# Optimization experiments

Hardware: AMD Instinct MI355X
Metric: run time of the kernel (lower is better)

The kernel has to match this reference:

```python
import jax, jax.numpy as jnp
import numpy as np

L_IN, L_K = 1, 1            # degree ranges (0..L)
C_IN, K_CH, H = 16, 8, 4    # in_channels, k_channels (per head), num_heads
C_OUT = H * K_CH            # 32
E, N_NODES, EMB = 32768, 4096, 64
M_IN, M_K = (L_IN + 1) ** 2, (L_K + 1) ** 2


def _so2_pairs(L_in, L_out):
    # enumerate SO(2)-equivariant weight blocks: for each order m, all (l_in, l_out)
    # pairs with l >= m; m=0 uses 1 matrix, m>0 uses 2 (real/imag parts).
    pairs, w = [], 0
    for m in range(min(L_in, L_out) + 1):
        for l_in in range(m, L_in + 1):
            for l_out in range(m, L_out + 1):
                pairs.append((m, l_in, l_out, w))
                w += 1 if m == 0 else 2
    return pairs, w

_PAIRS, NUM_W = _so2_pairs(L_IN, L_K)  # NUM_W = 6 for L_in=L_k=1


def so2_linear(x, W, L_in, L_out):
    # x: [E, (L_in+1)^2, Cin]; W: [NUM_W, Cin, Cout] (shared) or [E, NUM_W, Cin, Cout] (per-edge)
    per_edge = (W.ndim == 4)
    Cout = W.shape[-1]
    out = jnp.zeros((x.shape[0], (L_out + 1) ** 2, Cout), x.dtype)

    def mat(xs, w):
        return jnp.einsum('ec,eco->eo', xs, W[:, w]) if per_edge else xs @ W[w]

    pairs, _ = _so2_pairs(L_in, L_out)
    for m, l_in, l_out, w in pairs:
        i_in, i_out = l_in * (l_in + 1), l_out * (l_out + 1)  # flat index of (l, m=0)
        if m == 0:
            out = out.at[:, i_out].add(mat(x[:, i_in], w))
        else:
            xp, xn = x[:, i_in + m], x[:, i_in - m]
            out = out.at[:, i_out + m].add(mat(xp, w) - mat(xn, w + 1))
            out = out.at[:, i_out - m].add(mat(xp, w + 1) + mat(xn, w))
    return out


def segment_softmax(z, index, num_segments):
    # PyG-style softmax over ragged neighborhoods (max is detached, as in PyG)
    zmax = jax.lax.stop_gradient(jax.ops.segment_max(z, index, num_segments=num_segments))
    e = jnp.exp(z - zmax[index])
    denom = jax.ops.segment_sum(e, index, num_segments=num_segments)
    return e / denom[index]


def setup_inputs() -> dict:
    key = jax.random.key(0)
    ks = jax.random.split(key, 6)
    x_q = jax.random.normal(ks[0], (E, M_IN, C_IN), jnp.float32)
    x_k = jax.random.normal(ks[1], (E, M_IN, C_IN), jnp.float32)
    edge_emb = jax.random.normal(ks[2], (E, EMB), jnp.float32)
    index = jnp.sort(jax.random.randint(ks[3], (E,), 0, N_NODES))
    W_q = jax.random.normal(ks[4], (NUM_W, C_IN, C_OUT), jnp.float32) / np.sqrt(C_IN)
    W_p = jax.random.normal(ks[5], (EMB, NUM_W * C_IN * C_OUT), jnp.float32) / np.sqrt(EMB)
    return {"x_q": x_q, "x_k": x_k, "edge_emb": edge_emb, "index": index,
            "W_q": W_q, "W_p": W_p, "num_nodes": N_NODES}


def reference(x_q, x_k, edge_emb, index, W_q, W_p, num_nodes):
    # q_ij = W_Q x_i ; static SO2 weights
    q = so2_linear(x_q, W_q, L_IN, L_K).reshape(-1, M_K, H, K_CH)
    # k_ij = W_K(||r_ij||) x_j ; per-edge dynamic SO2 weights from edge embedding
    W_k = (edge_emb @ W_p).reshape(-1, NUM_W, C_IN, C_OUT)
    k = so2_linear(x_k, W_k, L_IN, L_K).reshape(-1, M_K, H, K_CH)
    scale = (K_CH // H) ** (-0.5)  # faithful to original: (k_channels // num_heads)**-0.5
    z = (q * k).sum((-1, -3)) * scale  # [E, H]
    return segment_softmax(z, index, num_nodes)
```

## Files before the change

### kernel.cpp

```cpp
#include <hip/hip_runtime.h>
#include <math.h>

#define E_TOTAL 32768
#define NUM_NODES 4096
#define SCALE 0.70710678118654752f

typedef __attribute__((ext_vector_type(8))) short bfrag;
typedef __attribute__((ext_vector_type(16))) float facc;

__device__ inline unsigned short f2bf(float f) {
  unsigned int u = __float_as_uint(f);
  unsigned int r = (u + 0x7FFFu + ((u >> 16) & 1u)) >> 16;
  return (unsigned short)r;
}
__device__ inline float bf2f(unsigned short s) {
  return __uint_as_float(((unsigned int)s) << 16);
}
__device__ inline void cvt8(const float* v, bfrag& hi, bfrag& lo) {
#pragma unroll
  for (int i = 0; i < 8; ++i) {
    unsigned short h = f2bf(v[i]);
    hi[i] = (short)h;
    lo[i] = (short)f2bf(v[i] - bf2f(h));
  }
}

__global__ __launch_bounds__(256) void prep_kernel(
    const float* __restrict__ Wp, const float* __restrict__ Wq,
    const int* __restrict__ index,
    unsigned short* __restrict__ fragWp, unsigned short* __restrict__ fragWq,
    int* __restrict__ offs)
{
  const int b = blockIdx.x, t = threadIdx.x;
  if (b < 96) {
    __shared__ unsigned short lds[4096];
    const int c = b / 6, w = b - c * 6;
    const int colbase = w * 512 + c * 32;
    const int cl = t & 31, dg = t >> 5;
#pragma unroll
    for (int i = 0; i < 8; ++i) {
      const int d = dg * 8 + i;
      const float v = Wp[(size_t)d * 3072 + colbase + cl];
      const unsigned short hi = f2bf(v);
      const unsigned short lo = f2bf(v - bf2f(hi));
      const int ks = d >> 4;
      const int lane = ((d >> 3) & 1) * 32 + cl;
      const int j = d & 7;
      lds[(ks * 2 + 0) * 512 + lane * 8 + j] = hi;
      lds[(ks * 2 + 1) * 512 + lane * 8 + j] = lo;
    }
    __syncthreads();
    unsigned short* dst = fragWp + (size_t)b * 4096;
    ((uint4*)dst)[t] = ((const uint4*)lds)[t];
    ((uint4*)dst)[t + 256] = ((const uint4*)lds)[t + 256];
  } else if (b < 103) {
    const int slot = b - 96;
    const int w = (slot == 6) ? 5 : slot;
    const float sgn = (slot == 6) ? -1.f : 1.f;
    for (int tt = t; tt < 512; tt += 256) {
      const int lane = tt >> 3, j = tt & 7;
      const int o = lane & 31, c = (lane >> 5) * 8 + j;
      const float v = sgn * Wq[(size_t)(w * 16 + c) * 32 + o];
      const unsigned short hi = f2bf(v);
      const unsigned short lo = f2bf(v - bf2f(hi));
      fragWq[slot * 1024 + lane * 8 + j] = hi;
      fragWq[slot * 1024 + 512 + lane * 8 + j] = lo;
    }
  } else {
    const int tg = (b - 103) * 256 + t;
    if (tg >= E_TOTAL) return;
    const int cur = index[tg];
    const int prev = (tg == 0) ? -1 : index[tg - 1];
    for (int n = prev + 1; n <= cur; ++n) offs[n] = tg;
    if (tg == E_TOTAL - 1)
      for (int n = cur + 1; n <= NUM_NODES; ++n) offs[n] = E_TOTAL;
  }
}

__global__ __launch_bounds__(256, 1) void main_kernel(
    const float* __restrict__ x_q, const float* __restrict__ x_k,
    const float* __restrict__ emb,
    const unsigned short* __restrict__ fragWp,
    const unsigned short* __restrict__ fragWq,
    float* __restrict__ z)
{
  __shared__ float xk_t[64][129];

  const int t = threadIdx.x;
  const int lane = t & 63, wv = t >> 6;
  const int col = lane & 31, half = lane >> 5;
  const int eb = blockIdx.x * 128;
  const int el = wv * 32 + col;
  const int e = eb + el;

  {
    const int er = t & 127, dh = (t >> 7) * 32;
    const float* src = x_k + (size_t)(eb + er) * 64 + dh;
#pragma unroll
    for (int i = 0; i < 8; ++i) {
      float4 v = *(const float4*)(src + i * 4);
      xk_t[dh + i * 4 + 0][er] = v.x;
      xk_t[dh + i * 4 + 1][er] = v.y;
      xk_t[dh + i * 4 + 2][er] = v.z;
      xk_t[dh + i * 4 + 3][er] = v.w;
    }
  }

  bfrag ebh[4], ebl[4];
#pragma unroll
  for (int ks = 0; ks < 4; ++ks) {
    float tmp[8];
    *(float4*)&tmp[0] = *(const float4*)(emb + (size_t)e * 64 + ks * 16 + half * 8);
    *(float4*)&tmp[4] = *(const float4*)(emb + (size_t)e * 64 + ks * 16 + half * 8 + 4);
    cvt8(tmp, ebh[ks], ebl[ks]);
  }

  facc ka0 = {0}, ka1 = {0}, ka2 = {0}, ka3 = {0};

  const unsigned short* fbase = fragWp + lane * 8;

  bfrag curh[4], curl[4], nxth[4], nxtl[4];
#pragma unroll
  for (int ks = 0; ks < 4; ++ks) {
    *(uint4*)&curh[ks] = *(const uint4*)(fbase + ks * 1024);
    *(uint4*)&curl[ks] = *(const uint4*)(fbase + ks * 1024 + 512);
  }

  __syncthreads();

  float xkc0 = 0.f, xkc1 = 0.f, xkc2 = 0.f, xkc3 = 0.f;

  for (int ot = 0; ot < 4; ++ot) {
#pragma unroll 6
    for (int ii = 0; ii < 24; ++ii) {
      const int it = ot * 24 + ii;
      const int j = ii % 6;
      {
        const int itn = (it < 95) ? it + 1 : 95;
        const unsigned short* gp = fbase + (size_t)itn * 4096;
#pragma unroll
        for (int ks = 0; ks < 4; ++ks) {
          *(uint4*)&nxth[ks] = *(const uint4*)(gp + ks * 1024);
          *(uint4*)&nxtl[ks] = *(const uint4*)(gp + ks * 1024 + 512);
        }
      }
      if (j == 0) {
        const int c16 = it / 6;
        xkc0 = xk_t[c16][el];
        xkc1 = xk_t[16 + c16][el];
        xkc2 = xk_t[32 + c16][el];
        xkc3 = xk_t[48 + c16][el];
      }
      facc cc0 = {0.f}, cc1 = {0.f}, cc2 = {0.f};
#pragma unroll
      for (int ks = 0; ks < 4; ++ks) {
        cc0 = __builtin_amdgcn_mfma_f32_32x32x16_bf16(curh[ks], ebh[ks], cc0, 0, 0, 0);
        cc1 = __builtin_amdgcn_mfma_f32_32x32x16_bf16(curh[ks], ebl[ks], cc1, 0, 0, 0);
        cc2 = __builtin_amdgcn_mfma_f32_32x32x16_bf16(curl[ks], ebh[ks], cc2, 0, 0, 0);
      }
      if (j < 4) {
        const float xv = (j & 2) ? xkc2 : xkc0;
        facc& kd = (j & 1) ? ka2 : ka0;
#pragma unroll
        for (int r = 0; r < 16; ++r)
          kd[r] = fmaf(xv, cc0[r] + cc1[r] + cc2[r], kd[r]);
      } else if (j == 4) {
#pragma unroll
        for (int r = 0; r < 16; ++r) {
          const float s = cc0[r] + cc1[r] + cc2[r];
          ka1[r] = fmaf(xkc1, s, ka1[r]);
          ka3[r] = fmaf(xkc3, s, ka3[r]);
        }
      } else {
#pragma unroll
        for (int r = 0; r < 16; ++r) {
          const float s = cc0[r] + cc1[r] + cc2[r];
          ka1[r] = fmaf(xkc3, s, ka1[r]);
          ka3[r] = fmaf(-xkc1, s, ka3[r]);
        }
      }
#pragma unroll
      for (int ks = 0; ks < 4; ++ks) { curh[ks] = nxth[ks]; curl[ks] = nxtl[ks]; }
    }
    __syncthreads();
  }

  bfrag xqh[4], xql[4];
#pragma unroll
  for (int a = 0; a < 4; ++a) {
    float tmp[8];
    *(float4*)&tmp[0] = *(const float4*)(x_q + (size_t)e * 64 + a * 16 + half * 8);
    *(float4*)&tmp[4] = *(const float4*)(x_q + (size_t)e * 64 + a * 16 + half * 8 + 4);
    cvt8(tmp, xqh[a], xql[a]);
  }
  float zp0 = 0.f, zp1 = 0.f, zp2 = 0.f, zp3 = 0.f;
  const int QA1[4] = {0, 1, 0, 3}, QS1[4] = {0, 4, 1, 4};
  const int QA2[4] = {2, 3, 2, 1}, QS2[4] = {2, 5, 3, 6};
#pragma unroll
  for (int m = 0; m < 4; ++m) {
    facc qa = {0.f};
#pragma unroll
    for (int tm = 0; tm < 2; ++tm) {
      const int a = tm ? QA2[m] : QA1[m];
      const int sl = tm ? QS2[m] : QS1[m];
      bfrag wh, wl;
      *(uint4*)&wh = *(const uint4*)(fragWq + sl * 1024 + lane * 8);
      *(uint4*)&wl = *(const uint4*)(fragWq + sl * 1024 + 512 + lane * 8);
      qa = __builtin_amdgcn_mfma_f32_32x32x16_bf16(wh, xqh[a], qa, 0, 0, 0);
      qa = __builtin_amdgcn_mfma_f32_32x32x16_bf16(wh, xql[a], qa, 0, 0, 0);
      qa = __builtin_amdgcn_mfma_f32_32x32x16_bf16(wl, xqh[a], qa, 0, 0, 0);
    }
    const facc& km = (m == 0) ? ka0 : (m == 1) ? ka1 : (m == 2) ? ka2 : ka3;
#pragma unroll
    for (int r = 0; r < 16; ++r) {
      const float v = qa[r] * km[r];
      if (r < 4) zp0 += v;
      else if (r < 8) zp1 += v;
      else if (r < 12) zp2 += v;
      else zp3 += v;
    }
  }
  zp0 += __shfl_xor(zp0, 32);
  zp1 += __shfl_xor(zp1, 32);
  zp2 += __shfl_xor(zp2, 32);
  zp3 += __shfl_xor(zp3, 32);
  if (half == 0) {
    float4 v = {zp0 * SCALE, zp1 * SCALE, zp2 * SCALE, zp3 * SCALE};
    *(float4*)&z[(size_t)e * 4] = v;
  }
}

__global__ __launch_bounds__(256) void softmax_kernel(
    const float* __restrict__ z, const int* __restrict__ offs,
    float* __restrict__ out)
{
  const int node = blockIdx.x * 4 + (threadIdx.x >> 6);
  const int lane = threadIdx.x & 63;
  const int start = offs[node], end = offs[node + 1];
  if (start >= end) return;
  const int h = lane & 3, eo = lane >> 2;
  float m = -INFINITY;
  for (int e = start + eo; e < end; e += 16) m = fmaxf(m, z[(size_t)e * 4 + h]);
#pragma unroll
  for (int s = 4; s < 64; s <<= 1) m = fmaxf(m, __shfl_xor(m, s));
  float sum = 0.f;
  for (int e = start + eo; e < end; e += 16) sum += __expf(z[(size_t)e * 4 + h] - m);
#pragma unroll
  for (int s = 4; s < 64; s <<= 1) sum += __shfl_xor(sum, s);
  const float inv = 1.f / sum;
  for (int e = start + eo; e < end; e += 16)
    out[(size_t)e * 4 + h] = __expf(z[(size_t)e * 4 + h] - m) * inv;
}

extern "C" void kernel_launch(void* const* d_in, const int* in_sizes, int n_in,
                              void* d_out, int out_size, void* d_ws, size_t ws_size,
                              hipStream_t stream) {
  const float* x_q = (const float*)d_in[0];
  const float* x_k = (const float*)d_in[1];
  const float* emb = (const float*)d_in[2];
  const int* index = (const int*)d_in[3];
  const float* W_q = (const float*)d_in[4];
  const float* W_p = (const float*)d_in[5];
  float* out = (float*)d_out;

  char* ws = (char*)d_ws;
  float* z = (float*)ws;
  int* offs = (int*)(ws + 524288);
  unsigned short* fragWp = (unsigned short*)(ws + 524288 + 32768);
  unsigned short* fragWq = (unsigned short*)(ws + 524288 + 32768 + 786432);

  prep_kernel<<<231, 256, 0, stream>>>(W_p, W_q, index, fragWp, fragWq, offs);
  main_kernel<<<256, 256, 0, stream>>>(x_q, x_k, emb, fragWp, fragWq, z);
  softmax_kernel<<<1024, 256, 0, stream>>>(z, offs, out);
}
```

Measured before the change: 124.7 us.

## Stage shared weight fragments into a double-buffered LDS via global_load_lds

```diff
diff --git a/kernel.cpp b/kernel.cpp
--- a/kernel.cpp
+++ b/kernel.cpp
@@ -23,6 +23,12 @@
     hi[i] = (short)h;
     lo[i] = (short)f2bf(v[i] - bf2f(h));
   }
+}
+
+__device__ inline void stage16(const void* g, void* l) {
+  __builtin_amdgcn_global_load_lds(
+      (const __attribute__((address_space(1))) unsigned int*)g,
+      (__attribute__((address_space(3))) unsigned int*)l, 16, 0, 0);
 }
 
 __global__ __launch_bounds__(256) void prep_kernel(
@@ -85,6 +91,7 @@
     float* __restrict__ z)
 {
   __shared__ float xk_t[64][129];
+  __shared__ alignas(16) unsigned short wbuf[2][4096];
 
   const int t = threadIdx.x;
   const int lane = t & 63, wv = t >> 6;
@@ -106,6 +113,13 @@
     }
   }
 
+  {
+    const char* tb = (const char*)fragWp;
+    char* db = (char*)&wbuf[0][0];
+    stage16(tb + (wv * 2 + 0) * 1024 + lane * 16, db + (wv * 2 + 0) * 1024);
+    stage16(tb + (wv * 2 + 1) * 1024 + lane * 16, db + (wv * 2 + 1) * 1024);
+  }
+
   bfrag ebh[4], ebl[4];
 #pragma unroll
   for (int ks = 0; ks < 4; ++ks) {
@@ -117,54 +131,47 @@
 
   facc ka0 = {0}, ka1 = {0}, ka2 = {0}, ka3 = {0};
 
-  const unsigned short* fbase = fragWp + lane * 8;
-
-  bfrag curh[4], curl[4], nxth[4], nxtl[4];
-#pragma unroll
-  for (int ks = 0; ks < 4; ++ks) {
-    *(uint4*)&curh[ks] = *(const uint4*)(fbase + ks * 1024);
-    *(uint4*)&curl[ks] = *(const uint4*)(fbase + ks * 1024 + 512);
-  }
-
   __syncthreads();
 
   float xkc0 = 0.f, xkc1 = 0.f, xkc2 = 0.f, xkc3 = 0.f;
 
-  for (int ot = 0; ot < 4; ++ot) {
-#pragma unroll 6
-    for (int ii = 0; ii < 24; ++ii) {
-      const int it = ot * 24 + ii;
-      const int j = ii % 6;
-      {
-        const int itn = (it < 95) ? it + 1 : 95;
-        const unsigned short* gp = fbase + (size_t)itn * 4096;
-#pragma unroll
-        for (int ks = 0; ks < 4; ++ks) {
-          *(uint4*)&nxth[ks] = *(const uint4*)(gp + ks * 1024);
-          *(uint4*)&nxtl[ks] = *(const uint4*)(gp + ks * 1024 + 512);
-        }
-      }
-      if (j == 0) {
-        const int c16 = it / 6;
-        xkc0 = xk_t[c16][el];
-        xkc1 = xk_t[16 + c16][el];
-        xkc2 = xk_t[32 + c16][el];
-        xkc3 = xk_t[48 + c16][el];
+  for (int ot = 0; ot < 16; ++ot) {
+#pragma unroll
+    for (int ii = 0; ii < 6; ++ii) {
+      const int it = ot * 6 + ii;
+      if (it != 95) {
+        const char* tb = (const char*)fragWp + (size_t)(it + 1) * 8192;
+        char* db = (char*)&wbuf[(ii + 1) & 1][0];
+        stage16(tb + (wv * 2 + 0) * 1024 + lane * 16, db + (wv * 2 + 0) * 1024);
+        stage16(tb + (wv * 2 + 1) * 1024 + lane * 16, db + (wv * 2 + 1) * 1024);
+      }
+      if (ii == 0) {
+        xkc0 = xk_t[ot][el];
+        xkc1 = xk_t[16 + ot][el];
+        xkc2 = xk_t[32 + ot][el];
+        xkc3 = xk_t[48 + ot][el];
+      }
+      const unsigned short* wb = &wbuf[ii & 1][0];
+      bfrag ch[4], cl4[4];
+#pragma unroll
+      for (int ks = 0; ks < 4; ++ks) {
+        *(uint4*)&ch[ks]  = *(const uint4*)(wb + ks * 1024 + lane * 8);
+        *(uint4*)&cl4[ks] = *(const uint4*)(wb + ks * 1024 + 512 + lane * 8);
       }
       facc cc0 = {0.f}, cc1 = {0.f}, cc2 = {0.f};
 #pragma unroll
       for (int ks = 0; ks < 4; ++ks) {
-        cc0 = __builtin_amdgcn_mfma_f32_32x32x16_bf16(curh[ks], ebh[ks], cc0, 0, 0, 0);
-        cc1 = __builtin_amdgcn_mfma_f32_32x32x16_bf16(curh[ks], ebl[ks], cc1, 0, 0, 0);
-        cc2 = __builtin_amdgcn_mfma_f32_32x32x16_bf16(curl[ks], ebh[ks], cc2, 0, 0, 0);
-      }
-      if (j < 4) {
-        const float xv = (j & 2) ? xkc2 : xkc0;
-        facc& kd = (j & 1) ? ka2 : ka0;
+        cc0 = __builtin_amdgcn_mfma_f32_32x32x16_bf16(ch[ks], ebh[ks], cc0, 0, 0, 0);
+        cc1 = __builtin_amdgcn_mfma_f32_32x32x16_bf16(ch[ks], ebl[ks], cc1, 0, 0, 0);
+        cc2 = __builtin_amdgcn_mfma_f32_32x32x16_bf16(cl4[ks], ebh[ks], cc2, 0, 0, 0);
+      }
+      if (ii < 4) {
+        const float xv = (ii & 2) ? xkc2 : xkc0;
+        facc& kd = (ii & 1) ? ka2 : ka0;
 #pragma unroll
         for (int r = 0; r < 16; ++r)
           kd[r] = fmaf(xv, cc0[r] + cc1[r] + cc2[r], kd[r]);
-      } else if (j == 4) {
+      } else if (ii == 4) {
 #pragma unroll
         for (int r = 0; r < 16; ++r) {
           const float s = cc0[r] + cc1[r] + cc2[r];
@@ -179,10 +186,8 @@
           ka3[r] = fmaf(-xkc1, s, ka3[r]);
         }
       }
-#pragma unroll
-      for (int ks = 0; ks < 4; ++ks) { curh[ks] = nxth[ks]; curl[ks] = nxtl[ks]; }
-    }
-    __syncthreads();
+      __syncthreads();
+    }
   }
 
   bfrag xqh[4], xql[4];
```

Measured after the change: 145.9 us. 1.17x slower.

## Split SO2 output orders across wave pairs, reuse weight fragments for two edge groups

Applied to the files above, without the earlier changes.

```diff
diff --git a/kernel.cpp b/kernel.cpp
--- a/kernel.cpp
+++ b/kernel.cpp
@@ -7,6 +7,8 @@
 
 typedef __attribute__((ext_vector_type(8))) short bfrag;
 typedef __attribute__((ext_vector_type(16))) float facc;
+
+#define MFMA __builtin_amdgcn_mfma_f32_32x32x16_bf16
 
 __device__ inline unsigned short f2bf(float f) {
   unsigned int u = __float_as_uint(f);
@@ -50,7 +52,9 @@
       lds[(ks * 2 + 1) * 512 + lane * 8 + j] = lo;
     }
     __syncthreads();
-    unsigned short* dst = fragWp + (size_t)b * 4096;
+    const int wslot0 = (w == 0) ? 0 : (w == 1) ? 64 : (w == 2) ? 16
+                     : (w == 3) ? 80 : (w == 4) ? 32 : 48;
+    unsigned short* dst = fragWp + (size_t)(wslot0 + c) * 4096;
     ((uint4*)dst)[t] = ((const uint4*)lds)[t];
     ((uint4*)dst)[t + 256] = ((const uint4*)lds)[t + 256];
   } else if (b < 103) {
@@ -85,13 +89,16 @@
     float* __restrict__ z)
 {
   __shared__ float xk_t[64][129];
+  __shared__ float zred[4][64][4];
 
   const int t = threadIdx.x;
   const int lane = t & 63, wv = t >> 6;
+  const int pr = wv & 1, pairI = wv >> 1;
   const int col = lane & 31, half = lane >> 5;
   const int eb = blockIdx.x * 128;
-  const int el = wv * 32 + col;
-  const int e = eb + el;
+  const int el0 = pairI * 64 + col;
+  const int el1 = el0 + 32;
+  const int e0 = eb + el0, e1 = eb + el1;
 
   {
     const int er = t & 127, dh = (t >> 7) * 32;
@@ -106,127 +113,131 @@
     }
   }
 
-  bfrag ebh[4], ebl[4];
+  bfrag ebh0[4], ebl0[4], ebh1[4], ebl1[4];
 #pragma unroll
   for (int ks = 0; ks < 4; ++ks) {
     float tmp[8];
-    *(float4*)&tmp[0] = *(const float4*)(emb + (size_t)e * 64 + ks * 16 + half * 8);
-    *(float4*)&tmp[4] = *(const float4*)(emb + (size_t)e * 64 + ks * 16 + half * 8 + 4);
-    cvt8(tmp, ebh[ks], ebl[ks]);
-  }
-
-  facc ka0 = {0}, ka1 = {0}, ka2 = {0}, ka3 = {0};
-
-  const unsigned short* fbase = fragWp + lane * 8;
-
-  bfrag curh[4], curl[4], nxth[4], nxtl[4];
-#pragma unroll
-  for (int ks = 0; ks < 4; ++ks) {
-    *(uint4*)&curh[ks] = *(const uint4*)(fbase + ks * 1024);
-    *(uint4*)&curl[ks] = *(const uint4*)(fbase + ks * 1024 + 512);
-  }
+    *(float4*)&tmp[0] = *(const float4*)(emb + (size_t)e0 * 64 + ks * 16 + half * 8);
+    *(float4*)&tmp[4] = *(const float4*)(emb + (size_t)e0 * 64 + ks * 16 + half * 8 + 4);
+    cvt8(tmp, ebh0[ks], ebl0[ks]);
+    *(float4*)&tmp[0] = *(const float4*)(emb + (size_t)e1 * 64 + ks * 16 + half * 8);
+    *(float4*)&tmp[4] = *(const float4*)(emb + (size_t)e1 * 64 + ks * 16 + half * 8 + 4);
+    cvt8(tmp, ebh1[ks], ebl1[ks]);
+  }
+
+  facc kaP0 = {0}, kaQ0 = {0}, kaP1 = {0}, kaQ1 = {0};
 
   __syncthreads();
 
-  float xkc0 = 0.f, xkc1 = 0.f, xkc2 = 0.f, xkc3 = 0.f;
-
-  for (int ot = 0; ot < 4; ++ot) {
-#pragma unroll 6
-    for (int ii = 0; ii < 24; ++ii) {
-      const int it = ot * 24 + ii;
-      const int j = ii % 6;
-      {
-        const int itn = (it < 95) ? it + 1 : 95;
-        const unsigned short* gp = fbase + (size_t)itn * 4096;
-#pragma unroll
-        for (int ks = 0; ks < 4; ++ks) {
-          *(uint4*)&nxth[ks] = *(const uint4*)(gp + ks * 1024);
-          *(uint4*)&nxtl[ks] = *(const uint4*)(gp + ks * 1024 + 512);
-        }
-      }
-      if (j == 0) {
-        const int c16 = it / 6;
-        xkc0 = xk_t[c16][el];
-        xkc1 = xk_t[16 + c16][el];
-        xkc2 = xk_t[32 + c16][el];
-        xkc3 = xk_t[48 + c16][el];
-      }
-      facc cc0 = {0.f}, cc1 = {0.f}, cc2 = {0.f};
-#pragma unroll
-      for (int ks = 0; ks < 4; ++ks) {
-        cc0 = __builtin_amdgcn_mfma_f32_32x32x16_bf16(curh[ks], ebh[ks], cc0, 0, 0, 0);
-        cc1 = __builtin_amdgcn_mfma_f32_32x32x16_bf16(curh[ks], ebl[ks], cc1, 0, 0, 0);
-        cc2 = __builtin_amdgcn_mfma_f32_32x32x16_bf16(curl[ks], ebh[ks], cc2, 0, 0, 0);
-      }
-      if (j < 4) {
-        const float xv = (j & 2) ? xkc2 : xkc0;
-        facc& kd = (j & 1) ? ka2 : ka0;
-#pragma unroll
-        for (int r = 0; r < 16; ++r)
-          kd[r] = fmaf(xv, cc0[r] + cc1[r] + cc2[r], kd[r]);
-      } else if (j == 4) {
-#pragma unroll
-        for (int r = 0; r < 16; ++r) {
-          const float s = cc0[r] + cc1[r] + cc2[r];
-          ka1[r] = fmaf(xkc1, s, ka1[r]);
-          ka3[r] = fmaf(xkc3, s, ka3[r]);
-        }
-      } else {
-#pragma unroll
-        for (int r = 0; r < 16; ++r) {
-          const float s = cc0[r] + cc1[r] + cc2[r];
-          ka1[r] = fmaf(xkc3, s, ka1[r]);
-          ka3[r] = fmaf(-xkc1, s, ka3[r]);
-        }
-      }
-#pragma unroll
-      for (int ks = 0; ks < 4; ++ks) { curh[ks] = nxth[ks]; curl[ks] = nxtl[ks]; }
-    }
-    __syncthreads();
-  }
-
-  bfrag xqh[4], xql[4];
-#pragma unroll
-  for (int a = 0; a < 4; ++a) {
-    float tmp[8];
-    *(float4*)&tmp[0] = *(const float4*)(x_q + (size_t)e * 64 + a * 16 + half * 8);
-    *(float4*)&tmp[4] = *(const float4*)(x_q + (size_t)e * 64 + a * 16 + half * 8 + 4);
-    cvt8(tmp, xqh[a], xql[a]);
-  }
-  float zp0 = 0.f, zp1 = 0.f, zp2 = 0.f, zp3 = 0.f;
-  const int QA1[4] = {0, 1, 0, 3}, QS1[4] = {0, 4, 1, 4};
-  const int QA2[4] = {2, 3, 2, 1}, QS2[4] = {2, 5, 3, 6};
-#pragma unroll
-  for (int m = 0; m < 4; ++m) {
-    facc qa = {0.f};
-#pragma unroll
-    for (int tm = 0; tm < 2; ++tm) {
-      const int a = tm ? QA2[m] : QA1[m];
-      const int sl = tm ? QS2[m] : QS1[m];
-      bfrag wh, wl;
-      *(uint4*)&wh = *(const uint4*)(fragWq + sl * 1024 + lane * 8);
-      *(uint4*)&wl = *(const uint4*)(fragWq + sl * 1024 + 512 + lane * 8);
-      qa = __builtin_amdgcn_mfma_f32_32x32x16_bf16(wh, xqh[a], qa, 0, 0, 0);
-      qa = __builtin_amdgcn_mfma_f32_32x32x16_bf16(wh, xql[a], qa, 0, 0, 0);
-      qa = __builtin_amdgcn_mfma_f32_32x32x16_bf16(wl, xqh[a], qa, 0, 0, 0);
-    }
-    const facc& km = (m == 0) ? ka0 : (m == 1) ? ka1 : (m == 2) ? ka2 : ka3;
+  const unsigned short* fb = fragWp + lane * 8;
+  const int qb0 = (pr ? 64 : 0) * 4096;
+  const int qb1 = (pr ? 80 : 16) * 4096;
+  const int qb2 = 32 * 4096;
+  const int qb3 = 48 * 4096;
+  const int r2 = pr ? 48 : 16;
+  const int r3 = pr ? 16 : 48;
+  const float sg3 = pr ? -1.f : 1.f;
+
+#define TILE(WB, XA, XB, KA, KB)                                              \
+  {                                                                           \
+    const unsigned short* wb_ = (WB);                                         \
+    bfrag fh[4], fl[4];                                                       \
+    _Pragma("unroll")                                                         \
+    for (int ks = 0; ks < 4; ++ks) {                                          \
+      *(uint4*)&fh[ks] = *(const uint4*)(wb_ + ks * 1024);                    \
+      *(uint4*)&fl[ks] = *(const uint4*)(wb_ + ks * 1024 + 512);              \
+    }                                                                         \
+    facc cc = {0.f}, cd = {0.f};                                              \
+    _Pragma("unroll")                                                         \
+    for (int ks = 0; ks < 4; ++ks) {                                          \
+      cc = MFMA(fh[ks], ebh0[ks], cc, 0, 0, 0);                               \
+      cd = MFMA(fh[ks], ebh1[ks], cd, 0, 0, 0);                               \
+      cc = MFMA(fh[ks], ebl0[ks], cc, 0, 0, 0);                               \
+      cd = MFMA(fh[ks], ebl1[ks], cd, 0, 0, 0);                               \
+      cc = MFMA(fl[ks], ebh0[ks], cc, 0, 0, 0);                               \
+      cd = MFMA(fl[ks], ebh1[ks], cd, 0, 0, 0);                               \
+    }                                                                         \
+    _Pragma("unroll")                                                         \
+    for (int r = 0; r < 16; ++r) {                                            \
+      (KA)[r] = fmaf((XA), cc[r], (KA)[r]);                                   \
+      (KB)[r] = fmaf((XB), cd[r], (KB)[r]);                                   \
+    }                                                                         \
+  }
+
+  for (int c = 0; c < 16; ++c) {
+    const float xs0a = xk_t[c][el0],          xs0b = xk_t[c][el1];
+    const float xs1a = xk_t[32 + c][el0],     xs1b = xk_t[32 + c][el1];
+    const float xs2a = xk_t[r2 + c][el0],     xs2b = xk_t[r2 + c][el1];
+    const float xs3a = sg3 * xk_t[r3 + c][el0], xs3b = sg3 * xk_t[r3 + c][el1];
+    TILE(fb + qb0 + c * 4096, xs0a, xs0b, kaP0, kaP1)
+    TILE(fb + qb1 + c * 4096, xs1a, xs1b, kaP0, kaP1)
+    TILE(fb + qb2 + c * 4096, xs2a, xs2b, kaQ0, kaQ1)
+    TILE(fb + qb3 + c * 4096, xs3a, xs3b, kaQ0, kaQ1)
+  }
+#undef TILE
+
+#define QTERM(QA_, A_, S_)                                                    \
+  {                                                                           \
+    bfrag wh, wl;                                                             \
+    *(uint4*)&wh = *(const uint4*)(fragWq + (S_)*1024 + lane * 8);            \
+    *(uint4*)&wl = *(const uint4*)(fragWq + (S_)*1024 + 512 + lane * 8);      \
+    QA_ = MFMA(wh, xqh[A_], QA_, 0, 0, 0);                                    \
+    QA_ = MFMA(wh, xql[A_], QA_, 0, 0, 0);                                    \
+    QA_ = MFMA(wl, xqh[A_], QA_, 0, 0, 0);                                    \
+  }
+
+#pragma unroll
+  for (int blk = 0; blk < 2; ++blk) {
+    const int e = blk ? e1 : e0;
+    bfrag xqh[4], xql[4];
+#pragma unroll
+    for (int a = 0; a < 4; ++a) {
+      float tmp[8];
+      *(float4*)&tmp[0] = *(const float4*)(x_q + (size_t)e * 64 + a * 16 + half * 8);
+      *(float4*)&tmp[4] = *(const float4*)(x_q + (size_t)e * 64 + a * 16 + half * 8 + 4);
+      cvt8(tmp, xqh[a], xql[a]);
+    }
+    facc qaP = {0.f}, qaQ = {0.f};
+    if (pr == 0) {
+      QTERM(qaP, 0, 0) QTERM(qaP, 2, 2)
+      QTERM(qaQ, 1, 4) QTERM(qaQ, 3, 5)
+    } else {
+      QTERM(qaP, 0, 1) QTERM(qaP, 2, 3)
+      QTERM(qaQ, 3, 4) QTERM(qaQ, 1, 6)
+    }
+    const facc& kp = blk ? kaP1 : kaP0;
+    const facc& kq = blk ? kaQ1 : kaQ0;
+    float zp0 = 0.f, zp1 = 0.f, zp2 = 0.f, zp3 = 0.f;
 #pragma unroll
     for (int r = 0; r < 16; ++r) {
-      const float v = qa[r] * km[r];
+      const float v = qaP[r] * kp[r] + qaQ[r] * kq[r];
       if (r < 4) zp0 += v;
       else if (r < 8) zp1 += v;
       else if (r < 12) zp2 += v;
       else zp3 += v;
     }
-  }
-  zp0 += __shfl_xor(zp0, 32);
-  zp1 += __shfl_xor(zp1, 32);
-  zp2 += __shfl_xor(zp2, 32);
-  zp3 += __shfl_xor(zp3, 32);
-  if (half == 0) {
-    float4 v = {zp0 * SCALE, zp1 * SCALE, zp2 * SCALE, zp3 * SCALE};
-    *(float4*)&z[(size_t)e * 4] = v;
+    zp0 += __shfl_xor(zp0, 32);
+    zp1 += __shfl_xor(zp1, 32);
+    zp2 += __shfl_xor(zp2, 32);
+    zp3 += __shfl_xor(zp3, 32);
+    if (half == 0) {
+      float4 v = {zp0, zp1, zp2, zp3};
+      *(float4*)&zred[wv][blk * 32 + col][0] = v;
+    }
+  }
+#undef QTERM
+
+  __syncthreads();
+  if (pr == 0 && half == 0) {
+#pragma unroll
+    for (int blk = 0; blk < 2; ++blk) {
+      const int idx = blk * 32 + col;
+      float4 a = *(const float4*)&zred[wv][idx][0];
+      float4 b = *(const float4*)&zred[wv ^ 1][idx][0];
+      float4 o = {(a.x + b.x) * SCALE, (a.y + b.y) * SCALE,
+                  (a.z + b.z) * SCALE, (a.w + b.w) * SCALE};
+      *(float4*)&z[(size_t)(eb + pairI * 64 + idx) * 4] = o;
+    }
   }
 }
 
```

Result: slower. 134.4 us (+7.8%).
